# Kernel optimization log

Measured on AMD Instinct MI355X. Metric: run time of the kernel, lower is better.

Reference implementation:

```python
import jax, jax.numpy as jnp
import numpy as np

B, N, D, H = 16, 576, 1024, 16
HD = D // H


def make_rel_indices(num_patches):
    # ConViT rel_indices: [N, N, 3] = (dx, dy, dx^2+dy^2) on a sqrt(N) grid
    img = int(num_patches ** 0.5)
    coords = np.arange(img)
    ind = coords.reshape(1, -1) - coords.reshape(-1, 1)  # [img, img]
    indx = np.tile(ind, (img, img))                      # repeats within rows
    indy = np.repeat(np.repeat(ind, img, axis=0), img, axis=1)
    indd = indx ** 2 + indy ** 2
    rel = np.stack([indx, indy, indd], axis=-1).astype(np.float32)  # [N, N, 3]
    return jnp.asarray(rel)


def setup_inputs() -> dict:
    key = jax.random.key(0)
    ks = jax.random.split(key, 8)
    s = D ** -0.5
    return {
        "x": jax.random.normal(ks[0], (B, N, D), jnp.float32),
        "W_qk": jax.random.normal(ks[1], (D, 2 * D), jnp.float32) * s,
        "W_v": jax.random.normal(ks[2], (D, D), jnp.float32) * s,
        "W_proj": jax.random.normal(ks[3], (D, D), jnp.float32) * s,
        "b_proj": jnp.zeros((D,), jnp.float32),
        "W_pos": jax.random.normal(ks[4], (3, H), jnp.float32) * 0.5,
        "b_pos": jnp.zeros((H,), jnp.float32),
        "gating": jnp.ones((H,), jnp.float32),
        "rel_indices": make_rel_indices(N),
    }


def reference(x, W_qk, W_v, W_proj, b_proj, W_pos, b_pos, gating, rel_indices):
    scale = HD ** -0.5
    qk = x @ W_qk                                  # [B, N, 2D]
    q = qk[..., :D].reshape(B, N, H, HD).transpose(0, 2, 1, 3)  # [B,H,N,HD]
    k = qk[..., D:].reshape(B, N, H, HD).transpose(0, 2, 1, 3)
    # content attention
    patch_score = jax.nn.softmax(jnp.einsum('bhnd,bhmd->bhnm', q, k) * scale, axis=-1)
    # learned positional attention from relative coordinates
    pos_logits = rel_indices @ W_pos + b_pos       # [N, N, H]
    pos_score = jax.nn.softmax(jnp.transpose(pos_logits, (2, 0, 1))[None], axis=-1)  # [1,H,N,N]
    # per-head gating mix, renormalized
    g = jax.nn.sigmoid(gating)[None, :, None, None]
    attn = (1.0 - g) * patch_score + g * pos_score
    attn = attn / attn.sum(axis=-1, keepdims=True)
    v = (x @ W_v).reshape(B, N, H, HD).transpose(0, 2, 1, 3)    # [B,H,N,HD]
    out = jnp.einsum('bhnm,bhmd->bhnd', attn, v)
    out = out.transpose(0, 2, 1, 3).reshape(B, N, D)
    return out @ W_proj + b_proj
```

## Files before the change

kernel.cpp:

```cpp
#include <hip/hip_runtime.h>
#include <hip/hip_bf16.h>
#include <math.h>

#define B_ 16
#define N_ 576
#define D_ 1024
#define H_ 16
#define HD_ 64
#define BN_ (B_ * N_)
#define LOG2E 1.4426950408889634f

typedef __bf16 bf16x8 __attribute__((ext_vector_type(8)));
typedef __bf16 bf16x4 __attribute__((ext_vector_type(4)));
typedef float  f32x4  __attribute__((ext_vector_type(4)));

__global__ __launch_bounds__(256) void cast_bf16(
    const float* __restrict__ in, __bf16* __restrict__ out)
{
    size_t i = ((size_t)blockIdx.x * 256 + threadIdx.x) * 4;
    float4 v = *(const float4*)&in[i];
    bf16x4 o;
    o.x = (__bf16)v.x; o.y = (__bf16)v.y; o.z = (__bf16)v.z; o.w = (__bf16)v.w;
    *(bf16x4*)&out[i] = o;
}

__global__ __launch_bounds__(256) void transpose_cast(
    const float* __restrict__ W, __bf16* __restrict__ Wt, int K, int N)
{
    __shared__ float t[64][65];
    const int tid = threadIdx.x;
    const int k0 = blockIdx.y * 64, n0 = blockIdx.x * 64;
    const int r = tid >> 4, c4 = (tid & 15) << 2;
#pragma unroll
    for (int s = 0; s < 4; ++s) {
        int rr = r + (s << 4);
        float4 w = *(const float4*)&W[(size_t)(k0 + rr) * N + n0 + c4];
        t[rr][c4] = w.x; t[rr][c4 + 1] = w.y; t[rr][c4 + 2] = w.z; t[rr][c4 + 3] = w.w;
    }
    __syncthreads();
#pragma unroll
    for (int s = 0; s < 4; ++s) {
        int rr = r + (s << 4);
        bf16x4 o;
        o.x = (__bf16)t[c4 + 0][rr]; o.y = (__bf16)t[c4 + 1][rr];
        o.z = (__bf16)t[c4 + 2][rr]; o.w = (__bf16)t[c4 + 3][rr];
        *(bf16x4*)&Wt[(size_t)(n0 + rr) * K + k0 + c4] = o;
    }
}

template<int OUTMODE>
__global__ __launch_bounds__(256) void gemm_mfma(
    const __bf16* __restrict__ A, const __bf16* __restrict__ Bt,
    const float* __restrict__ bias, void* __restrict__ Cp, void* __restrict__ Cp2,
    int M, int N, int K)
{
    __shared__ __bf16 As[128 * 32];
    __shared__ __bf16 Bs[128 * 32];
    const int tid  = threadIdx.x;
    const int lane = tid & 63;
    const int wave = tid >> 6;
    const int m0 = blockIdx.y * 128;
    const int n0 = blockIdx.x * 128;
    const int wm = (wave >> 1) * 64;
    const int wn = (wave & 1) * 64;

    const int r0 = tid >> 2, q0 = tid & 3;
    const int qs0 = q0 ^ ((r0 >> 1) & 3);
    const int r1 = r0 + 64;
    const int qs1 = q0 ^ ((r1 >> 1) & 3);
    const __bf16* srcA0 = A  + (size_t)(m0 + r0) * K + qs0 * 8;
    const __bf16* srcA1 = A  + (size_t)(m0 + r1) * K + qs1 * 8;
    const __bf16* srcB0 = Bt + (size_t)(n0 + r0) * K + qs0 * 8;
    const __bf16* srcB1 = Bt + (size_t)(n0 + r1) * K + qs1 * 8;
    __bf16* dstA0 = &As[(wave * 64) * 8];
    __bf16* dstA1 = &As[(256 + wave * 64) * 8];
    __bf16* dstB0 = &Bs[(wave * 64) * 8];
    __bf16* dstB1 = &Bs[(256 + wave * 64) * 8];

    const int fr = lane & 15, quad = lane >> 4;
    int aoff[4], boff[4];
#pragma unroll
    for (int i = 0; i < 4; ++i) {
        int row = wm + i * 16 + fr;
        aoff[i] = row * 32 + (quad ^ ((row >> 1) & 3)) * 8;
    }
#pragma unroll
    for (int j = 0; j < 4; ++j) {
        int row = wn + j * 16 + fr;
        boff[j] = row * 32 + (quad ^ ((row >> 1) & 3)) * 8;
    }

    f32x4 acc[4][4];
#pragma unroll
    for (int i = 0; i < 4; ++i)
#pragma unroll
        for (int j = 0; j < 4; ++j)
            acc[i][j] = (f32x4){0.f, 0.f, 0.f, 0.f};

    for (int k0 = 0; k0 < K; k0 += 32) {
        __syncthreads();
        __builtin_amdgcn_global_load_lds(
            (const __attribute__((address_space(1))) void*)(srcA0 + k0),
            (__attribute__((address_space(3))) void*)dstA0, 16, 0, 0);
        __builtin_amdgcn_global_load_lds(
            (const __attribute__((address_space(1))) void*)(srcA1 + k0),
            (__attribute__((address_space(3))) void*)dstA1, 16, 0, 0);
        __builtin_amdgcn_global_load_lds(
            (const __attribute__((address_space(1))) void*)(srcB0 + k0),
            (__attribute__((address_space(3))) void*)dstB0, 16, 0, 0);
        __builtin_amdgcn_global_load_lds(
            (const __attribute__((address_space(1))) void*)(srcB1 + k0),
            (__attribute__((address_space(3))) void*)dstB1, 16, 0, 0);
        __syncthreads();

        bf16x8 af[4], bfv[4];
#pragma unroll
        for (int i = 0; i < 4; ++i) af[i]  = *(const bf16x8*)&As[aoff[i]];
#pragma unroll
        for (int j = 0; j < 4; ++j) bfv[j] = *(const bf16x8*)&Bs[boff[j]];
#pragma unroll
        for (int i = 0; i < 4; ++i)
#pragma unroll
            for (int j = 0; j < 4; ++j)
                acc[i][j] = __builtin_amdgcn_mfma_f32_16x16x32_bf16(
                    af[i], bfv[j], acc[i][j], 0, 0, 0);
    }

    const int colb = n0 + wn + fr;
    const int rowb = m0 + wm + quad * 4;
#pragma unroll
    for (int j = 0; j < 4; ++j) {
        int col = colb + j * 16;
        float bv = (OUTMODE == 0 && bias) ? bias[col] : 0.0f;
#pragma unroll
        for (int i = 0; i < 4; ++i) {
            int row = rowb + i * 16;
            if (OUTMODE == 3) {
                if (col < 2048) {
#pragma unroll
                    for (int t = 0; t < 4; ++t)
                        ((__bf16*)Cp)[(size_t)(row + t) * 2048 + col] = (__bf16)acc[i][j][t];
                } else {
                    int bb = row / 576;
                    int ml = row - bb * 576;
                    bf16x4 o4;
#pragma unroll
                    for (int t = 0; t < 4; ++t) o4[t] = (__bf16)acc[i][j][t];
                    *(bf16x4*)&((__bf16*)Cp2)[((size_t)bb * 1024 + (col - 2048)) * 576 + ml] = o4;
                }
            } else {
#pragma unroll
                for (int t = 0; t < 4; ++t) {
                    float v = acc[i][j][t] + bv;
                    if (OUTMODE == 1) ((__bf16*)Cp)[(size_t)(row + t) * N + col] = (__bf16)v;
                    else              ((float*)Cp)[(size_t)(row + t) * N + col] = v;
                }
            }
        }
    }
}

__global__ __launch_bounds__(64) void pos_mat(
    const float* __restrict__ W_pos, const float* __restrict__ gating,
    __bf16* __restrict__ Pp)
{
    const int h = blockIdx.x / N_;
    const int n = blockIdx.x % N_;
    const int lane = threadIdx.x;
    const float w0 = W_pos[h] * LOG2E, w1 = W_pos[H_ + h] * LOG2E,
                w2 = W_pos[2 * H_ + h] * LOG2E;
    const float rx = (float)(n % 24), ry = (float)(n / 24);
    float l2[9];
    float mx = -1e30f;
#pragma unroll
    for (int i = 0; i < 9; ++i) {
        int m = lane + (i << 6);
        float cx = (float)(m % 24), cy = (float)(m / 24);
        float dx = cx - rx, dy = cy - ry;
        float l = fmaf(w2, fmaf(dx, dx, dy * dy), fmaf(w0, dx, w1 * dy));
        l2[i] = l;
        mx = fmaxf(mx, l);
    }
#pragma unroll
    for (int off = 32; off; off >>= 1) mx = fmaxf(mx, __shfl_xor(mx, off, 64));
    float sum = 0.f;
#pragma unroll
    for (int i = 0; i < 9; ++i) sum += __builtin_amdgcn_exp2f(l2[i] - mx);
#pragma unroll
    for (int off = 32; off; off >>= 1) sum += __shfl_xor(sum, off, 64);
    float g = 1.f / (1.f + __expf(-gating[h]));
    float c = __log2f(g) - mx - __log2f(sum);
    __bf16* row = Pp + (size_t)(h * N_ + n) * N_;
#pragma unroll
    for (int i = 0; i < 9; ++i)
        row[(i << 6) + lane] = (__bf16)__builtin_amdgcn_exp2f(l2[i] + c);
}

__global__ __launch_bounds__(512, 2) void attn_mfma3(
    const __bf16* __restrict__ qk, const __bf16* __restrict__ vt,
    const __bf16* __restrict__ Pp, const float* __restrict__ gating,
    __bf16* __restrict__ ao)
{
    __shared__ __bf16 Ks[N_ * HD_];
    __shared__ __bf16 Vs[HD_ * N_];
    __shared__ __bf16 Sc[8 * 16 * 56];

    const int bid = blockIdx.x;
    const int h = bid & 15, b = bid >> 4;
    const int tid = threadIdx.x;
    const int lane = tid & 63, wave = tid >> 6;
    const int fr = lane & 15, quad = lane >> 4;

    const __bf16* qbase = qk + (size_t)b * N_ * (2 * D_) + h * HD_;
    const __bf16* kgl   = qbase + D_;
    const __bf16* vgl   = vt + (size_t)(b * H_ + h) * HD_ * N_;

#pragma unroll 3
    for (int it = 0; it < 9; ++it) {
        int s = it * 512 + tid;
        int r = s >> 3, p = s & 7;
        int l = p ^ (r & 7);
        __builtin_amdgcn_global_load_lds(
            (const __attribute__((address_space(1))) void*)(kgl + (size_t)r * (2 * D_) + l * 8),
            (__attribute__((address_space(3))) void*)&Ks[(size_t)(it * 512 + wave * 64) * 8],
            16, 0, 0);
        int d = s / 72, pv = s - d * 72;
        int lv = (pv & ~7) | ((pv & 7) ^ (d & 7));
        __builtin_amdgcn_global_load_lds(
            (const __attribute__((address_space(1))) void*)(vgl + (size_t)d * N_ + lv * 8),
            (__attribute__((address_space(3))) void*)&Vs[(size_t)(it * 512 + wave * 64) * 8],
            16, 0, 0);
    }
    __syncthreads();

    const float g   = 1.f / (1.f + __expf(-gating[h]));
    const float omg = 1.f - g;
    const float kk = 0.125f * LOG2E;

    __bf16* sw = &Sc[wave * 16 * 56];

    for (int tt = wave; tt < 36; tt += 8) {
        const int n0 = tt * 16;

        const __bf16* qp = qbase + (size_t)(n0 + fr) * (2 * D_) + quad * 8;
        bf16x8 qf0 = *(const bf16x8*)qp;
        bf16x8 qf1 = *(const bf16x8*)(qp + 32);

        const __bf16* pprow = Pp + ((size_t)h * N_ + n0 + fr) * N_ + quad * 8;

        f32x4 S[36];
#pragma unroll
        for (int ct = 0; ct < 36; ++ct) {
            int row = ct * 16 + fr;
            int p0 = quad ^ (row & 7);
            int p1 = (4 + quad) ^ (row & 7);
            bf16x8 k0 = *(const bf16x8*)&Ks[row * 64 + p0 * 8];
            bf16x8 k1 = *(const bf16x8*)&Ks[row * 64 + p1 * 8];
            f32x4 a = (f32x4){0.f, 0.f, 0.f, 0.f};
            a = __builtin_amdgcn_mfma_f32_16x16x32_bf16(qf0, k0, a, 0, 0, 0);
            a = __builtin_amdgcn_mfma_f32_16x16x32_bf16(qf1, k1, a, 0, 0, 0);
            S[ct] = a;
        }

        float inv[4];
#pragma unroll
        for (int t = 0; t < 4; ++t) {
            float mt[18];
#pragma unroll
            for (int i = 0; i < 18; ++i) mt[i] = fmaxf(S[i][t], S[i + 18][t]);
#pragma unroll
            for (int i = 0; i < 9; ++i) mt[i] = fmaxf(mt[i], mt[i + 9]);
            float m = fmaxf(fmaxf(fmaxf(mt[0], mt[1]), fmaxf(mt[2], mt[3])),
                            fmaxf(fmaxf(fmaxf(mt[4], mt[5]), fmaxf(mt[6], mt[7])), mt[8]));
            m = fmaxf(m, __shfl_xor(m, 1, 16));
            m = fmaxf(m, __shfl_xor(m, 2, 16));
            m = fmaxf(m, __shfl_xor(m, 4, 16));
            m = fmaxf(m, __shfl_xor(m, 8, 16));
            float km = kk * m;
            float s0 = 0.f, s1 = 0.f, s2 = 0.f, s3 = 0.f;
#pragma unroll
            for (int ct = 0; ct < 36; ++ct) {
                float e = __builtin_amdgcn_exp2f(fmaf(kk, S[ct][t], -km));
                S[ct][t] = e;
                if ((ct & 3) == 0)      s0 += e;
                else if ((ct & 3) == 1) s1 += e;
                else if ((ct & 3) == 2) s2 += e;
                else                    s3 += e;
            }
            float s = (s0 + s1) + (s2 + s3);
            s += __shfl_xor(s, 1, 16);
            s += __shfl_xor(s, 2, 16);
            s += __shfl_xor(s, 4, 16);
            s += __shfl_xor(s, 8, 16);
            inv[t] = omg / s;
        }

        f32x4 O[4];
#pragma unroll
        for (int dt = 0; dt < 4; ++dt) O[dt] = (f32x4){0.f, 0.f, 0.f, 0.f};
#pragma unroll
        for (int kb = 0; kb < 18; ++kb) {
            bf16x8 posf = *(const bf16x8*)(pprow + kb * 32);
#pragma unroll
            for (int ctl = 0; ctl < 2; ++ctl) {
                int ct = 2 * kb + ctl;
#pragma unroll
                for (int t = 0; t < 4; ++t) {
                    float pval = S[ct][t] * inv[t];
                    sw[(quad * 4 + t) * 56 + ctl * 16 + fr] = (__bf16)pval;
                }
            }
            bf16x8 pf = *(const bf16x8*)&sw[fr * 56 + quad * 8];
#pragma unroll
            for (int dt = 0; dt < 4; ++dt) {
                int d = dt * 16 + fr;
                int l = kb * 4 + quad;
                int p = (l & ~7) | ((l & 7) ^ (d & 7));
                bf16x8 vf = *(const bf16x8*)&Vs[d * 576 + p * 8];
                O[dt] = __builtin_amdgcn_mfma_f32_16x16x32_bf16(vf, pf,   O[dt], 0, 0, 0);
                O[dt] = __builtin_amdgcn_mfma_f32_16x16x32_bf16(vf, posf, O[dt], 0, 0, 0);
            }
        }

        asm volatile("s_waitcnt lgkmcnt(0)" ::: "memory");
#pragma unroll
        for (int ps = 0; ps < 2; ++ps) {
#pragma unroll
            for (int dh = 0; dh < 2; ++dh) {
                int dt = 2 * ps + dh;
                bf16x4 o4;
#pragma unroll
                for (int t = 0; t < 4; ++t) o4[t] = (__bf16)O[dt][t];
                *(bf16x4*)&sw[fr * 56 + dh * 16 + quad * 4] = o4;
            }
            asm volatile("s_waitcnt lgkmcnt(0)" ::: "memory");
            {
                int row = lane >> 2;
                int off = (lane & 3) * 8;
                bf16x8 ov = *(const bf16x8*)&sw[row * 56 + off];
                *(bf16x8*)&ao[((size_t)b * N_ + n0 + row) * D_ + h * HD_ + ps * 32 + off] = ov;
            }
            asm volatile("s_waitcnt lgkmcnt(0)" ::: "memory");
        }
    }
}

extern "C" void kernel_launch(void* const* d_in, const int* in_sizes, int n_in,
                              void* d_out, int out_size, void* d_ws, size_t ws_size,
                              hipStream_t stream)
{
    const float* x      = (const float*)d_in[0];
    const float* W_qk   = (const float*)d_in[1];
    const float* W_v    = (const float*)d_in[2];
    const float* W_proj = (const float*)d_in[3];
    const float* b_proj = (const float*)d_in[4];
    const float* W_pos  = (const float*)d_in[5];
    const float* b_pos  = (const float*)d_in[6];
    const float* gating = (const float*)d_in[7];
    const float* rel    = (const float*)d_in[8];
    (void)b_pos; (void)rel;
    float* out = (float*)d_out;

    char* p = (char*)d_ws;
    __bf16* xb    = (__bf16*)p;  p += (size_t)BN_ * D_ * 2;
    __bf16* wqkvt = (__bf16*)p;  p += (size_t)(3 * D_) * D_ * 2;
    __bf16* wpt   = (__bf16*)p;  p += (size_t)D_ * D_ * 2;
    __bf16* qkb   = (__bf16*)p;  p += (size_t)BN_ * (2 * D_) * 2;
    __bf16* vt    = (__bf16*)p;  p += (size_t)BN_ * D_ * 2;
    __bf16* aob   = (__bf16*)p;  p += (size_t)BN_ * D_ * 2;
    __bf16* Pp    = (__bf16*)p;

    cast_bf16<<<(BN_ * D_) / 1024, 256, 0, stream>>>(x, xb);
    transpose_cast<<<dim3((2 * D_) / 64, D_ / 64), 256, 0, stream>>>(W_qk, wqkvt, D_, 2 * D_);
    transpose_cast<<<dim3(D_ / 64, D_ / 64), 256, 0, stream>>>(W_v, wqkvt + (size_t)2 * D_ * D_, D_, D_);
    transpose_cast<<<dim3(D_ / 64, D_ / 64), 256, 0, stream>>>(W_proj, wpt, D_, D_);

    gemm_mfma<3><<<dim3((3 * D_) / 128, BN_ / 128), 256, 0, stream>>>(
        xb, wqkvt, nullptr, qkb, vt, BN_, 3 * D_, D_);
    pos_mat<<<H_ * N_, 64, 0, stream>>>(W_pos, gating, Pp);
    attn_mfma3<<<B_ * H_, 512, 0, stream>>>(qkb, vt, Pp, gating, aob);
    gemm_mfma<0><<<dim3(D_ / 128, BN_ / 128), 256, 0, stream>>>(
        aob, wpt, b_proj, out, nullptr, BN_, D_, D_);
}
```

Before: 311.8 us.

## Replace GEMM with 256x256 double-buffered pipelined MFMA kernel and XCD-aware block remap

Replaces the 128x128 single-buffered GEMM with a 256x256-tile, 512-thread kernel that double-buffers K=64 slices in LDS. It interleaves global_load_lds issues with MFMA quarter-tiles behind explicit vmcnt waits and barriers, and raises wave priority around the MFMA blocks. Block indices are remapped across the 8 XCDs to improve L2 locality. The aim is to hide load latency and raise arithmetic intensity, at the cost of much more LDS (128KB) and register pressure, and of hardcoding K=1024.

```diff
diff --git a/kernel.cpp b/kernel.cpp
--- a/kernel.cpp
+++ b/kernel.cpp
@@ -49,82 +49,126 @@
 }
 
 template<int OUTMODE>
-__global__ __launch_bounds__(256) void gemm_mfma(
+__global__ __launch_bounds__(512, 2) void gemm256(
     const __bf16* __restrict__ A, const __bf16* __restrict__ Bt,
     const float* __restrict__ bias, void* __restrict__ Cp, void* __restrict__ Cp2,
-    int M, int N, int K)
-{
-    __shared__ __bf16 As[128 * 32];
-    __shared__ __bf16 Bs[128 * 32];
-    const int tid  = threadIdx.x;
-    const int lane = tid & 63;
-    const int wave = tid >> 6;
-    const int m0 = blockIdx.y * 128;
-    const int n0 = blockIdx.x * 128;
-    const int wm = (wave >> 1) * 64;
-    const int wn = (wave & 1) * 64;
-
-    const int r0 = tid >> 2, q0 = tid & 3;
-    const int qs0 = q0 ^ ((r0 >> 1) & 3);
-    const int r1 = r0 + 64;
-    const int qs1 = q0 ^ ((r1 >> 1) & 3);
-    const __bf16* srcA0 = A  + (size_t)(m0 + r0) * K + qs0 * 8;
-    const __bf16* srcA1 = A  + (size_t)(m0 + r1) * K + qs1 * 8;
-    const __bf16* srcB0 = Bt + (size_t)(n0 + r0) * K + qs0 * 8;
-    const __bf16* srcB1 = Bt + (size_t)(n0 + r1) * K + qs1 * 8;
-    __bf16* dstA0 = &As[(wave * 64) * 8];
-    __bf16* dstA1 = &As[(256 + wave * 64) * 8];
-    __bf16* dstB0 = &Bs[(wave * 64) * 8];
-    __bf16* dstB1 = &Bs[(256 + wave * 64) * 8];
-
+    int M, int N, int nbn)
+{
+    __shared__ __bf16 As[2][256 * 64];
+    __shared__ __bf16 Bs[2][256 * 64];
+
+    const int tid = threadIdx.x;
+    const int lane = tid & 63, wave = tid >> 6;
     const int fr = lane & 15, quad = lane >> 4;
-    int aoff[4], boff[4];
-#pragma unroll
-    for (int i = 0; i < 4; ++i) {
-        int row = wm + i * 16 + fr;
-        aoff[i] = row * 32 + (quad ^ ((row >> 1) & 3)) * 8;
-    }
-#pragma unroll
-    for (int j = 0; j < 4; ++j) {
-        int row = wn + j * 16 + fr;
-        boff[j] = row * 32 + (quad ^ ((row >> 1) & 3)) * 8;
-    }
-
-    f32x4 acc[4][4];
-#pragma unroll
-    for (int i = 0; i < 4; ++i)
+
+    const int nwg = gridDim.x;
+    const int wg = ((int)blockIdx.x & 7) * (nwg >> 3) + ((int)blockIdx.x >> 3);
+    const int m0 = (wg / nbn) * 256;
+    const int n0 = (wg % nbn) * 256;
+
+    const int wm = (wave >> 2) * 128;
+    const int wn = (wave & 3) * 64;
+
+    int offA[2], offB[2], dA[2], dB[2];
+#pragma unroll
+    for (int r = 0; r < 2; ++r) {
+        int rl = r * 64 + (tid >> 3);
+        int pc = tid & 7;
+        int l  = pc ^ (rl & 7);
+        int rowA = (rl & 63) | ((rl & 64) << 1);
+        int rowB = (rl & 31) + ((rl >> 5) << 6);
+        offA[r] = (m0 + rowA) * 1024 + l * 8;
+        offB[r] = (n0 + rowB) * 1024 + l * 8;
+        int rlb = r * 64 + wave * 8;
+        int rowAb = (rlb & 63) | ((rlb & 64) << 1);
+        int rowBb = (rlb & 31) + ((rlb >> 5) << 6);
+        dA[r] = rowAb * 64;
+        dB[r] = rowBb * 64;
+    }
+
+    const int cA0 = (quad ^ (fr & 7)) * 8;
+    const int cA1 = ((4 + quad) ^ (fr & 7)) * 8;
+
+    f32x4 acc[8][4];
+#pragma unroll
+    for (int i = 0; i < 8; ++i)
 #pragma unroll
         for (int j = 0; j < 4; ++j)
             acc[i][j] = (f32x4){0.f, 0.f, 0.f, 0.f};
 
-    for (int k0 = 0; k0 < K; k0 += 32) {
-        __syncthreads();
-        __builtin_amdgcn_global_load_lds(
-            (const __attribute__((address_space(1))) void*)(srcA0 + k0),
-            (__attribute__((address_space(3))) void*)dstA0, 16, 0, 0);
-        __builtin_amdgcn_global_load_lds(
-            (const __attribute__((address_space(1))) void*)(srcA1 + k0),
-            (__attribute__((address_space(3))) void*)dstA1, 16, 0, 0);
-        __builtin_amdgcn_global_load_lds(
-            (const __attribute__((address_space(1))) void*)(srcB0 + k0),
-            (__attribute__((address_space(3))) void*)dstB0, 16, 0, 0);
-        __builtin_amdgcn_global_load_lds(
-            (const __attribute__((address_space(1))) void*)(srcB1 + k0),
-            (__attribute__((address_space(3))) void*)dstB1, 16, 0, 0);
-        __syncthreads();
-
-        bf16x8 af[4], bfv[4];
-#pragma unroll
-        for (int i = 0; i < 4; ++i) af[i]  = *(const bf16x8*)&As[aoff[i]];
-#pragma unroll
-        for (int j = 0; j < 4; ++j) bfv[j] = *(const bf16x8*)&Bs[boff[j]];
-#pragma unroll
-        for (int i = 0; i < 4; ++i)
-#pragma unroll
-            for (int j = 0; j < 4; ++j)
-                acc[i][j] = __builtin_amdgcn_mfma_f32_16x16x32_bf16(
-                    af[i], bfv[j], acc[i][j], 0, 0, 0);
-    }
+    bf16x8 af[2][4];
+    bf16x8 bfr[2][2][2];
+
+#define GLL16(src, dst) __builtin_amdgcn_global_load_lds( \
+    (const __attribute__((address_space(1))) void*)(src), \
+    (__attribute__((address_space(3))) void*)(dst), 16, 0, 0)
+
+#define ISSUE_A(U, BUF, KOFF) { \
+    GLL16(A + offA[0] + (U) * 65536 + (KOFF), &As[BUF][dA[0] + (U) * 4096]); \
+    GLL16(A + offA[1] + (U) * 65536 + (KOFF), &As[BUF][dA[1] + (U) * 4096]); }
+#define ISSUE_B(U, BUF, KOFF) { \
+    GLL16(Bt + offB[0] + (U) * 32768 + (KOFF), &Bs[BUF][dB[0] + (U) * 2048]); \
+    GLL16(Bt + offB[1] + (U) * 32768 + (KOFF), &Bs[BUF][dB[1] + (U) * 2048]); }
+
+#define READ_A(BUF, MH) { \
+    const __bf16* _p = &As[BUF][(wm + (MH) * 64 + fr) * 64]; \
+    _Pragma("unroll") for (int i = 0; i < 4; ++i) { \
+        af[0][i] = *(const bf16x8*)&_p[i * 1024 + cA0]; \
+        af[1][i] = *(const bf16x8*)&_p[i * 1024 + cA1]; } }
+
+#define READ_B(BUF, NH) { \
+    const __bf16* _p = &Bs[BUF][(wn + (NH) * 32 + fr) * 64]; \
+    _Pragma("unroll") for (int j = 0; j < 2; ++j) { \
+        bfr[NH][0][j] = *(const bf16x8*)&_p[j * 1024 + cA0]; \
+        bfr[NH][1][j] = *(const bf16x8*)&_p[j * 1024 + cA1]; } }
+
+#define MFMAQ(MH, NH) { \
+    __builtin_amdgcn_s_setprio(1); \
+    _Pragma("unroll") for (int i = 0; i < 4; ++i) \
+    _Pragma("unroll") for (int j = 0; j < 2; ++j) { \
+        f32x4 c = acc[(MH) * 4 + i][(NH) * 2 + j]; \
+        c = __builtin_amdgcn_mfma_f32_16x16x32_bf16(af[0][i], bfr[NH][0][j], c, 0, 0, 0); \
+        c = __builtin_amdgcn_mfma_f32_16x16x32_bf16(af[1][i], bfr[NH][1][j], c, 0, 0, 0); \
+        acc[(MH) * 4 + i][(NH) * 2 + j] = c; } \
+    __builtin_amdgcn_s_setprio(0); }
+
+#define WAITV(N) asm volatile("s_waitcnt vmcnt(" #N ")" ::: "memory")
+#define BARL() { asm volatile("s_waitcnt lgkmcnt(0)" ::: "memory"); \
+                 asm volatile("s_barrier" ::: "memory"); }
+
+#define ITER(LAST) { \
+     ISSUE_A(0, 1, kodd); WAITV(4); BARL(); READ_A(0, 0); READ_B(0, 0); MFMAQ(0, 0); \
+     ISSUE_B(0, 1, kodd); WAITV(4); BARL(); READ_B(0, 1); MFMAQ(0, 1); \
+     ISSUE_A(1, 1, kodd); WAITV(4); BARL(); READ_A(0, 1); MFMAQ(1, 1); \
+     ISSUE_B(1, 1, kodd); WAITV(4); BARL(); MFMAQ(1, 0); \
+     if (!(LAST)) { ISSUE_A(0, 0, keven); } WAITV(4); BARL(); READ_A(1, 0); READ_B(1, 0); MFMAQ(0, 0); \
+     if (!(LAST)) { ISSUE_B(0, 0, keven); WAITV(4); } else { WAITV(0); } BARL(); READ_B(1, 1); MFMAQ(0, 1); \
+     if (!(LAST)) { ISSUE_A(1, 0, keven); WAITV(4); } BARL(); READ_A(1, 1); MFMAQ(1, 1); \
+     if (!(LAST)) { ISSUE_B(1, 0, keven); WAITV(4); } BARL(); MFMAQ(1, 0); }
+
+    ISSUE_A(0, 0, 0); ISSUE_B(0, 0, 0); ISSUE_A(1, 0, 0); ISSUE_B(1, 0, 0);
+
+#pragma unroll 1
+    for (int it = 0; it < 7; ++it) {
+        const int kodd  = it * 128 + 64;
+        const int keven = it * 128 + 128;
+        ITER(0);
+    }
+    {
+        const int kodd  = 7 * 128 + 64;
+        const int keven = 0;
+        ITER(1);
+    }
+
+#undef ITER
+#undef WAITV
+#undef BARL
+#undef MFMAQ
+#undef READ_B
+#undef READ_A
+#undef ISSUE_B
+#undef ISSUE_A
+#undef GLL16
 
     const int colb = n0 + wn + fr;
     const int rowb = m0 + wm + quad * 4;
@@ -133,7 +177,7 @@
         int col = colb + j * 16;
         float bv = (OUTMODE == 0 && bias) ? bias[col] : 0.0f;
 #pragma unroll
-        for (int i = 0; i < 4; ++i) {
+        for (int i = 0; i < 8; ++i) {
             int row = rowb + i * 16;
             if (OUTMODE == 3) {
                 if (col < 2048) {
@@ -150,11 +194,8 @@
                 }
             } else {
 #pragma unroll
-                for (int t = 0; t < 4; ++t) {
-                    float v = acc[i][j][t] + bv;
-                    if (OUTMODE == 1) ((__bf16*)Cp)[(size_t)(row + t) * N + col] = (__bf16)v;
-                    else              ((float*)Cp)[(size_t)(row + t) * N + col] = v;
-                }
+                for (int t = 0; t < 4; ++t)
+                    ((float*)Cp)[(size_t)(row + t) * N + col] = acc[i][j][t] + bv;
             }
         }
     }
@@ -375,10 +416,10 @@
     transpose_cast<<<dim3(D_ / 64, D_ / 64), 256, 0, stream>>>(W_v, wqkvt + (size_t)2 * D_ * D_, D_, D_);
     transpose_cast<<<dim3(D_ / 64, D_ / 64), 256, 0, stream>>>(W_proj, wpt, D_, D_);
 
-    gemm_mfma<3><<<dim3((3 * D_) / 128, BN_ / 128), 256, 0, stream>>>(
-        xb, wqkvt, nullptr, qkb, vt, BN_, 3 * D_, D_);
+    gemm256<3><<<dim3((BN_ / 256) * (3 * D_ / 256)), 512, 0, stream>>>(
+        xb, wqkvt, nullptr, qkb, vt, BN_, 3 * D_, 3 * D_ / 256);
     pos_mat<<<H_ * N_, 64, 0, stream>>>(W_pos, gating, Pp);
     attn_mfma3<<<B_ * H_, 512, 0, stream>>>(qkb, vt, Pp, gating, aob);
-    gemm_mfma<0><<<dim3(D_ / 128, BN_ / 128), 256, 0, stream>>>(
-        aob, wpt, b_proj, out, nullptr, BN_, D_, D_);
-}
+    gemm256<0><<<dim3((BN_ / 256) * (D_ / 256)), 512, 0, stream>>>(
+        aob, wpt, b_proj, out, nullptr, BN_, D_, D_ / 256);
+}
```

Result: faster. 287.5 us (-7.8%).
